# Kernel tuning notes

Measured on AMD Instinct MI355X. Metric: run time of the kernel, lower is better.

## Reference

```python
import jax, jax.numpy as jnp
import numpy as np

HIDDEN = 128
RHO = 5        # K // 2 with K = 10
J = 5
SCALE = 5.0


def setup_inputs() -> dict:
    key = jax.random.key(0)
    ks = jax.random.split(key, 16)
    B, N, D = 2, 4096, HIDDEN
    eigvs = jax.random.uniform(ks[0], (B, N, D), dtype=jnp.float32)  # eigenvalue encodings in [0,1)
    x = jax.random.normal(ks[1], (B, N, D), dtype=jnp.float32)
    U = jax.random.normal(ks[2], (B, N, N), dtype=jnp.float32) / np.sqrt(N)
    s = 1.0 / np.sqrt(D)
    return {
        "eigvs": eigvs, "x": x, "U": U,
        # Linear weights stored as [in, out] (already transposed vs torch)
        "Wa": jax.random.normal(ks[3], (D, RHO), dtype=jnp.float32) * s,
        "ba": jnp.zeros((RHO,), jnp.float32),
        "Wb": jax.random.normal(ks[4], (D, RHO), dtype=jnp.float32) * s,
        "bb": jnp.zeros((RHO,), jnp.float32),
        "Ws": jax.random.normal(ks[5], (D, J), dtype=jnp.float32) * s,
        "bs": jnp.zeros((J,), jnp.float32),
        "WS": jax.random.normal(ks[6], (D, D), dtype=jnp.float32) * s,
        "bS": jnp.zeros((D,), jnp.float32),
        "WM": jax.random.normal(ks[7], (J, D, D), dtype=jnp.float32) * s,
        "bM": jnp.zeros((J, D), jnp.float32),
        "Ww": jax.random.normal(ks[8], (D, D), dtype=jnp.float32) * s,
        "bw": jnp.zeros((D,), jnp.float32),
    }


def _generate_g(a, sx, rho):
    # a: [B, rho]; sx: [B, J, N, D] scaled eigenvalues. Even Chebyshev polys.
    T_odd = jnp.ones_like(sx)
    T_even = sx
    g = a[:, 0, None, None, None] * T_even
    for i in range(1, rho):
        T_odd = 2.0 * sx * T_even - T_odd
        T_even = 2.0 * sx * T_odd - T_even
        g = g + a[:, i, None, None, None] * T_even
    return g


def _generate_h(b, e, rho):
    # b: [B, rho]; e: [B, N, D]. Odd Chebyshev polys.
    T_odd = jnp.ones_like(e)
    T_even = e
    h = b[:, 0, None, None] * T_odd
    for i in range(1, rho):
        T_odd = 2.0 * e * T_even - T_odd
        T_even = 2.0 * e * T_odd - T_even
        h = h + b[:, i, None, None] * T_odd
    return h


def reference(eigvs, x, U, Wa, ba, Wb, bb, Ws, bs, WS, bS, WM, bM, Ww, bw):
    # Filter coefficients from pooled eigenvalue encodings
    a_tilde = (eigvs @ Wa + ba).mean(axis=-2)                      # [B, rho]
    b_tilde = (eigvs @ Wb + bb).mean(axis=-2)                      # [B, rho]
    scale_tilde = jax.nn.sigmoid((eigvs @ Ws + bs).mean(axis=-2)) * SCALE  # [B, J]

    h = _generate_h(b_tilde, eigvs, RHO)                           # [B, N, D] scaling filter
    sx = scale_tilde[:, :, None, None] * eigvs[:, None]            # [B, J, N, D]
    g = _generate_g(a_tilde, sx, RHO)                              # [B, J, N, D] wavelet filters

    # Spectral convolution: U diag(filter) U^T x, per channel
    xt = jnp.einsum('bmn,bmd->bnd', U, x)                          # U^T x
    y_h = jnp.einsum('bnm,bmd->bnd', U, h * xt)                    # [B, N, D]
    y_g = jnp.einsum('bnm,bjmd->bjnd', U, g * xt[:, None])         # [B, J, N, D]

    out = y_h @ WS + bS                                            # S_kernel
    out = out + jnp.einsum('bjnd,jde->bne', y_g, WM) + bM.sum(0)   # sum_j M_kernels[j]
    return out @ Ww + bw                                           # W
```

## Files before the change

### kernel.cpp

```cpp
#include <hip/hip_runtime.h>
#include <hip/hip_bf16.h>
#include <stdint.h>

typedef unsigned short u16;
typedef __attribute__((ext_vector_type(8))) short bf16x8;
typedef __attribute__((ext_vector_type(4))) float f32x4;
typedef __attribute__((ext_vector_type(4))) uint32_t u32x4;

__device__ inline u16 f2bf(float f) {
  union { float f; uint32_t u; } v; v.f = f;
  uint32_t u = v.u;
  u += 0x7FFFu + ((u >> 16) & 1u);
  return (u16)(u >> 16);
}

__device__ inline uint32_t pkbf(float a, float b) {
  union { __hip_bfloat162 h; uint32_t u; } c;
  c.h = __float22bfloat162_rn(float2{a, b});
  return c.u;
}

__device__ inline void gl_lds16(const void* g, void* s) {
  __builtin_amdgcn_global_load_lds(
      (const __attribute__((address_space(1))) void*)(uintptr_t)(g),
      (__attribute__((address_space(3))) void*)(uint32_t)(uintptr_t)(s),
      16, 0, 0);
}

__global__ void k_mean(const float* __restrict__ eig, float* __restrict__ part) {
  const int b = blockIdx.y, chunk = blockIdx.x;
  const int t = threadIdx.x, d = t & 127, half = t >> 7;
  const float* p = eig + ((long)b * 4096 + chunk * 128 + half) * 128 + d;
  float s = 0.0f;
  for (int i = 0; i < 64; i++) s += p[(long)i * 256];
  __shared__ float red[256];
  red[t] = s;
  __syncthreads();
  if (t < 128) part[((long)b * 32 + chunk) * 128 + d] = red[t] + red[t + 128];
}

__global__ void k_coeff(const float* __restrict__ part,
                        const float* __restrict__ Wa, const float* __restrict__ ba,
                        const float* __restrict__ Wb, const float* __restrict__ bb_,
                        const float* __restrict__ Ws, const float* __restrict__ bs,
                        float* __restrict__ coeff) {
  const int b = blockIdx.x, t = threadIdx.x;
  __shared__ float sd[128];
  float s = 0.0f;
  for (int c = 0; c < 32; c++) s += part[((long)b * 32 + c) * 128 + t];
  sd[t] = s * (1.0f / 4096.0f);
  __syncthreads();
  if (t >= 15) return;
  const int kind = t / 5, r = t % 5;
  const float* W = (kind == 0) ? Wa : ((kind == 1) ? Wb : Ws);
  float v = 0.0f;
  for (int d = 0; d < 128; d++) v += sd[d] * W[d * 5 + r];
  v += (kind == 0) ? ba[r] : ((kind == 1) ? bb_[r] : bs[r]);
  if (kind == 2) v = 5.0f / (1.0f + __expf(-v));
  coeff[b * 16 + kind * 5 + r] = v;
}

__global__ void k_fold(const float* __restrict__ WS, const float* __restrict__ WM,
                       const float* __restrict__ Ww, const float* __restrict__ bS,
                       const float* __restrict__ bM, const float* __restrict__ bw,
                       u16* __restrict__ VT, float* __restrict__ cvec) {
  const int q = blockIdx.x;
  const int e = threadIdx.x;
  if (q == 768) {
    float s = bw[e];
    for (int k = 0; k < 128; k++) {
      float t = bS[k];
#pragma unroll
      for (int j = 0; j < 5; j++) t += bM[j * 128 + k];
      s += t * Ww[k * 128 + e];
    }
    cvec[e] = s;
    return;
  }
  const int f = q >> 7, d = q & 127;
  const float* Frow = (f == 0) ? (WS + d * 128) : (WM + ((long)(f - 1) * 128 + d) * 128);
  float s = 0.0f;
  for (int k = 0; k < 128; k++) s += Frow[k] * Ww[k * 128 + e];
  VT[(long)e * 768 + f * 128 + d] = f2bf(s);
}

__global__ void k_filter(const float* __restrict__ eig, const float* __restrict__ xs,
                         const float* __restrict__ coeff, u16* __restrict__ Mod) {
  const int b = blockIdx.y;
  const int n = blockIdx.x * 2 + (threadIdx.x >> 7);
  const int d = threadIdx.x & 127;
  const long ridx = (long)b * 4096 + n;
  const long off = ridx * 128 + d;
  const float e = eig[off];
  float xv = 0.0f;
#pragma unroll
  for (int s = 0; s < 8; s++) xv += xs[off + (long)s * 1048576];
  const float* cf = coeff + b * 16;
  float To = 1.0f, Tev = e;
  float h = cf[5];
#pragma unroll
  for (int i = 1; i < 5; i++) {
    To = 2.0f * e * Tev - To;
    Tev = 2.0f * e * To - Tev;
    h += cf[5 + i] * To;
  }
  u16* row = Mod + ridx * 768;
  row[d] = f2bf(h * xv);
#pragma unroll
  for (int j = 0; j < 5; j++) {
    const float sx = cf[10 + j] * e;
    float To2 = 1.0f, Te2 = sx;
    float g = cf[0] * Te2;
#pragma unroll
    for (int i = 1; i < 5; i++) {
      To2 = 2.0f * sx * Te2 - To2;
      Te2 = 2.0f * sx * To2 - Te2;
      g += cf[i] * Te2;
    }
    row[(j + 1) * 128 + d] = f2bf(g * xv);
  }
}

__global__ void k_wred(const float* __restrict__ wsl, u16* __restrict__ wT) {
  const long i = ((long)blockIdx.x * 256 + threadIdx.x) * 4;
  float4 s = *(const float4*)(wsl + i);
#pragma unroll
  for (int k = 1; k < 4; k++) {
    const float4 t = *(const float4*)(wsl + i + (long)k * 1048576);
    s.x += t.x; s.y += t.y; s.z += t.z; s.w += t.w;
  }
  uint32_t lo = pkbf(s.x, s.y), hi = pkbf(s.z, s.w);
  *(uint2*)(wT + i) = uint2{lo, hi};
}

__global__ void k_outred(const float* __restrict__ os, const float* __restrict__ cvec,
                         float* __restrict__ out) {
  const long i = (long)blockIdx.x * 256 + threadIdx.x;
  float4 r = *(const float4*)(os + 4 * i);
#pragma unroll
  for (int s = 1; s < 8; s++) {
    const float4 t = *(const float4*)(os + 4 * i + (long)s * 1048576);
    r.x += t.x; r.y += t.y; r.z += t.z; r.w += t.w;
  }
  const float4 cv = *(const float4*)(cvec + (i & 31) * 4);
  r.x += cv.x; r.y += cv.y; r.z += cv.z; r.w += cv.w;
  *(float4*)(out + 4 * i) = r;
}

__device__ inline void stage_t32(const float* __restrict__ srcK, int lda,
                                 u16* __restrict__ lds, int t) {
  const int q = t & 15, cb = t >> 4;
  const float* r0 = srcK + (long)(2 * q) * lda + cb * 8;
  const float* r1 = r0 + lda;
  const float4 a0 = *(const float4*)(r0);
  const float4 a1 = *(const float4*)(r0 + 4);
  const float4 b0 = *(const float4*)(r1);
  const float4 b1 = *(const float4*)(r1 + 4);
  uint32_t* d = (uint32_t*)lds;
  const int base = cb * 128 + q;
  d[base +   0] = pkbf(a0.x, b0.x);
  d[base +  16] = pkbf(a0.y, b0.y);
  d[base +  32] = pkbf(a0.z, b0.z);
  d[base +  48] = pkbf(a0.w, b0.w);
  d[base +  64] = pkbf(a1.x, b1.x);
  d[base +  80] = pkbf(a1.y, b1.y);
  d[base +  96] = pkbf(a1.z, b1.z);
  d[base + 112] = pkbf(a1.w, b1.w);
}

template <int AT, int BT>
__global__ __launch_bounds__(256) void k_gemm(
    const void* __restrict__ A, long sA, int lda,
    const void* __restrict__ B, long sB, int ldb,
    float* __restrict__ C, long sC, int ldc, long kslice,
    int K, int kchunk, int m_tiles) {
  __shared__ __align__(16) u16 As[128 * 32];
  __shared__ __align__(16) u16 Bs[128 * 32];
  const int bb = blockIdx.z, ks = blockIdx.y;
  const int tm = blockIdx.x % m_tiles, tn = blockIdx.x / m_tiles;
  const int tid = threadIdx.x, wave = tid >> 6, lane = tid & 63;
  const int wm = (wave >> 1) * 64, wn = (wave & 1) * 64;
  f32x4 acc[4][4];
#pragma unroll
  for (int i = 0; i < 4; i++)
#pragma unroll
    for (int j = 0; j < 4; j++)
#pragma unroll
      for (int r = 0; r < 4; r++) acc[i][j][r] = 0.0f;
  const int a_off = (wm + (lane & 15)) * 64 + (lane >> 4) * 16;
  const int b_off = (wn + (lane & 15)) * 64 + (lane >> 4) * 16;
  const int srow = wave * 32 + (lane >> 2);
  const int scol = (lane & 3) * 8;
  for (int k0 = 0; k0 < kchunk; k0 += 32) {
    const int kb = ks * kchunk + k0;
    if constexpr (AT == 0) {
      const u16* Ab = (const u16*)A + (long)bb * sA + (long)tm * 128 * lda + kb;
#pragma unroll
      for (int i = 0; i < 2; i++)
        gl_lds16(Ab + (long)(srow + i * 16) * lda + scol,
                 (char*)As + (wave * 32 + i * 16) * 64);
    } else if constexpr (AT == 1) {
      const float* src = (const float*)A + (long)bb * sA +
                         (long)(tm * 128 + (tid >> 1)) * lda + kb + (tid & 1) * 16;
      const float4 f0 = *(const float4*)(src);
      const float4 f1 = *(const float4*)(src + 4);
      const float4 f2 = *(const float4*)(src + 8);
      const float4 f3 = *(const float4*)(src + 12);
      u32x4* dst = (u32x4*)((char*)As + (tid >> 1) * 64 + (tid & 1) * 32);
      dst[0] = u32x4{pkbf(f0.x, f0.y), pkbf(f0.z, f0.w), pkbf(f1.x, f1.y), pkbf(f1.z, f1.w)};
      dst[1] = u32x4{pkbf(f2.x, f2.y), pkbf(f2.z, f2.w), pkbf(f3.x, f3.y), pkbf(f3.z, f3.w)};
    } else {
      const float* src = (const float*)A + (long)bb * sA + (long)kb * lda + tm * 128;
      stage_t32(src, lda, As, tid);
    }
    if constexpr (BT == 0) {
      const u16* Bb = (const u16*)B + (long)bb * sB + (long)tn * 128 * ldb + kb;
#pragma unroll
      for (int i = 0; i < 2; i++)
        gl_lds16(Bb + (long)(srow + i * 16) * ldb + scol,
                 (char*)Bs + (wave * 32 + i * 16) * 64);
    } else {
      const float* src = (const float*)B + (long)bb * sB + (long)kb * ldb + tn * 128;
      stage_t32(src, ldb, Bs, tid);
    }
    __syncthreads();
    bf16x8 af[4], bfr[4];
#pragma unroll
    for (int mt = 0; mt < 4; mt++)
      af[mt] = *(const bf16x8*)((const char*)As + a_off + mt * 1024);
#pragma unroll
    for (int nt = 0; nt < 4; nt++)
      bfr[nt] = *(const bf16x8*)((const char*)Bs + b_off + nt * 1024);
#pragma unroll
    for (int mt = 0; mt < 4; mt++)
#pragma unroll
      for (int nt = 0; nt < 4; nt++)
        acc[mt][nt] = __builtin_amdgcn_mfma_f32_16x16x32_bf16(af[mt], bfr[nt], acc[mt][nt], 0, 0, 0);
    __syncthreads();
  }
  const int lr = (lane >> 4) * 4, lc = lane & 15;
  float* Cf = C + (long)bb * sC + (long)ks * kslice;
#pragma unroll
  for (int mt = 0; mt < 4; mt++)
#pragma unroll
    for (int nt = 0; nt < 4; nt++) {
      const int col = tn * 128 + wn + nt * 16 + lc;
#pragma unroll
      for (int r = 0; r < 4; r++) {
        const int row = tm * 128 + wm + mt * 16 + lr + r;
        Cf[(long)row * ldc + col] = acc[mt][nt][r];
      }
    }
}

extern "C" void kernel_launch(void* const* d_in, const int* in_sizes, int n_in,
                              void* d_out, int out_size, void* d_ws, size_t ws_size,
                              hipStream_t stream) {
  const float* eig = (const float*)d_in[0];
  const float* x   = (const float*)d_in[1];
  const float* U   = (const float*)d_in[2];
  const float* Wa  = (const float*)d_in[3];
  const float* ba  = (const float*)d_in[4];
  const float* Wb  = (const float*)d_in[5];
  const float* bb  = (const float*)d_in[6];
  const float* Ws  = (const float*)d_in[7];
  const float* bs  = (const float*)d_in[8];
  const float* WSm = (const float*)d_in[9];
  const float* bS  = (const float*)d_in[10];
  const float* WM  = (const float*)d_in[11];
  const float* bM  = (const float*)d_in[12];
  const float* Ww  = (const float*)d_in[13];
  const float* bw  = (const float*)d_in[14];

  char* ws = (char*)d_ws;
  float* xs   = (float*)(ws + 0);
  u16*   Mod  = (u16*)(ws + 33554432);
  u16*   VT   = (u16*)(ws + 46137344);
  float* wsl  = (float*)(ws + 46333952);
  u16*   wT   = (u16*)(ws + 63111168);
  float* os   = (float*)(ws + 65208320);
  float* part = (float*)(ws + 98762752);
  float* coef = (float*)(ws + 98795520);
  float* cvec = (float*)(ws + 98795648);
  float* outp = (float*)d_out;

  if (ws_size < (size_t)98796160) return;

  k_mean<<<dim3(32, 2), 256, 0, stream>>>(eig, part);
  k_coeff<<<2, 128, 0, stream>>>(part, Wa, ba, Wb, bb, Ws, bs, coef);

  k_fold<<<769, 128, 0, stream>>>(WSm, WM, Ww, bS, bM, bw, VT, cvec);

  k_gemm<2, 2><<<dim3(32, 8, 2), 256, 0, stream>>>(
      U, 16777216L, 4096, x, 524288L, 128,
      xs, 524288L, 128, 1048576L, 4096, 512, 32);

  k_filter<<<dim3(2048, 2), 256, 0, stream>>>(eig, xs, coef, Mod);

  k_gemm<0, 0><<<dim3(32, 4, 2), 256, 0, stream>>>(
      VT, 0L, 768, Mod, 3145728L, 768,
      wsl, 524288L, 4096, 1048576L, 768, 192, 1);
  k_wred<<<1024, 256, 0, stream>>>(wsl, wT);

  k_gemm<1, 0><<<dim3(32, 8, 2), 256, 0, stream>>>(
      U, 16777216L, 4096, wT, 524288L, 4096,
      os, 524288L, 128, 1048576L, 4096, 512, 32);

  k_outred<<<1024, 256, 0, stream>>>(os, cvec, outp);
}
```

Baseline: 319.9 us.

## Pre-transpose x to bf16, read U row-major, drop split-K reduction and merge prep kernels

Adds a prep kernel that computes eigenvalue partial means and transposes x into bf16, so the first U^T x GEMM reads U as a row-major B operand through a padded LDS layout and writes its result transposed. The filter-weight GEMM drops split-K and writes bf16 directly, which removes the separate reduction kernel and its fp32 workspace traffic. The coefficient and weight-fold kernels are merged into one launch. The aim is fewer launches and less intermediate memory traffic, at the cost of lower parallelism in the unsplit GEMM.

```diff
diff --git a/kernel.cpp b/kernel.cpp
--- a/kernel.cpp
+++ b/kernel.cpp
@@ -27,45 +27,84 @@
       16, 0, 0);
 }
 
-__global__ void k_mean(const float* __restrict__ eig, float* __restrict__ part) {
-  const int b = blockIdx.y, chunk = blockIdx.x;
-  const int t = threadIdx.x, d = t & 127, half = t >> 7;
-  const float* p = eig + ((long)b * 4096 + chunk * 128 + half) * 128 + d;
-  float s = 0.0f;
-  for (int i = 0; i < 64; i++) s += p[(long)i * 256];
-  __shared__ float red[256];
-  red[t] = s;
+__global__ __launch_bounds__(256) void k_pre(const float* __restrict__ eig,
+                                             const float* __restrict__ x,
+                                             float* __restrict__ part,
+                                             u16* __restrict__ xT) {
+  const int bid = blockIdx.x, t = threadIdx.x;
+  if (bid < 64) {
+    const int b = bid >> 5, chunk = bid & 31;
+    const int d = t & 127, half = t >> 7;
+    const float* p = eig + ((long)b * 4096 + chunk * 128 + half) * 128 + d;
+    float s = 0.0f;
+    for (int i = 0; i < 64; i++) s += p[(long)i * 256];
+    __shared__ float red[256];
+    red[t] = s;
+    __syncthreads();
+    if (t < 128) part[((long)b * 32 + chunk) * 128 + d] = red[t] + red[t + 128];
+    return;
+  }
+  const int q = bid - 64;
+  const int b = q >> 7, rem = q & 127;
+  const int tr = rem & 63, tc = rem >> 6;
+  const float* I = x + (long)b * 524288;
+  u16* O = xT + (long)b * 524288;
+  __shared__ uint32_t L[64][33];
+  const int r = t >> 2, cq = (t & 3) * 4;
+  const float* src = I + (long)(tr * 64 + r) * 128 + tc * 64;
+#pragma unroll
+  for (int i = 0; i < 4; i++) {
+    const float4 f = *(const float4*)(src + cq + 16 * i);
+    const int c = cq + 16 * i;
+    L[r][(c >> 1)]     = pkbf(f.x, f.y);
+    L[r][(c >> 1) + 1] = pkbf(f.z, f.w);
+  }
   __syncthreads();
-  if (t < 128) part[((long)b * 32 + chunk) * 128 + d] = red[t] + red[t + 128];
-}
-
-__global__ void k_coeff(const float* __restrict__ part,
-                        const float* __restrict__ Wa, const float* __restrict__ ba,
-                        const float* __restrict__ Wb, const float* __restrict__ bb_,
-                        const float* __restrict__ Ws, const float* __restrict__ bs,
-                        float* __restrict__ coeff) {
-  const int b = blockIdx.x, t = threadIdx.x;
-  __shared__ float sd[128];
-  float s = 0.0f;
-  for (int c = 0; c < 32; c++) s += part[((long)b * 32 + c) * 128 + t];
-  sd[t] = s * (1.0f / 4096.0f);
-  __syncthreads();
-  if (t >= 15) return;
-  const int kind = t / 5, r = t % 5;
-  const float* W = (kind == 0) ? Wa : ((kind == 1) ? Wb : Ws);
-  float v = 0.0f;
-  for (int d = 0; d < 128; d++) v += sd[d] * W[d * 5 + r];
-  v += (kind == 0) ? ba[r] : ((kind == 1) ? bb_[r] : bs[r]);
-  if (kind == 2) v = 5.0f / (1.0f + __expf(-v));
-  coeff[b * 16 + kind * 5 + r] = v;
-}
-
-__global__ void k_fold(const float* __restrict__ WS, const float* __restrict__ WM,
-                       const float* __restrict__ Ww, const float* __restrict__ bS,
-                       const float* __restrict__ bM, const float* __restrict__ bw,
-                       u16* __restrict__ VT, float* __restrict__ cvec) {
-  const int q = blockIdx.x;
-  const int e = threadIdx.x;
+  const int r0 = (t & 7) * 8;
+#pragma unroll
+  for (int p = 0; p < 2; p++) {
+    const int c = (t >> 3) + 32 * p;
+    uint32_t w[4];
+#pragma unroll
+    for (int i = 0; i < 4; i++) {
+      const uint32_t w0 = L[r0 + 2 * i][c >> 1];
+      const uint32_t w1 = L[r0 + 2 * i + 1][c >> 1];
+      const u16 v0 = (c & 1) ? (u16)(w0 >> 16) : (u16)(w0 & 0xffff);
+      const u16 v1 = (c & 1) ? (u16)(w1 >> 16) : (u16)(w1 & 0xffff);
+      w[i] = (uint32_t)v0 | ((uint32_t)v1 << 16);
+    }
+    u32x4* dst = (u32x4*)(O + (long)(tc * 64 + c) * 4096 + tr * 64 + r0);
+    *dst = u32x4{w[0], w[1], w[2], w[3]};
+  }
+}
+
+__global__ void k_foldcoeff(const float* __restrict__ WS, const float* __restrict__ WM,
+                            const float* __restrict__ Ww, const float* __restrict__ bS,
+                            const float* __restrict__ bM, const float* __restrict__ bw,
+                            const float* __restrict__ part,
+                            const float* __restrict__ Wa, const float* __restrict__ ba,
+                            const float* __restrict__ Wb, const float* __restrict__ bb_,
+                            const float* __restrict__ Ws, const float* __restrict__ bs,
+                            u16* __restrict__ VT, float* __restrict__ cvec,
+                            float* __restrict__ coeff) {
+  const int q = blockIdx.x, e = threadIdx.x;
+  if (q >= 769) {
+    const int b = q - 769;
+    __shared__ float sd[128];
+    float s = 0.0f;
+    for (int c = 0; c < 32; c++) s += part[((long)b * 32 + c) * 128 + e];
+    sd[e] = s * (1.0f / 4096.0f);
+    __syncthreads();
+    if (e >= 15) return;
+    const int kind = e / 5, r = e % 5;
+    const float* W = (kind == 0) ? Wa : ((kind == 1) ? Wb : Ws);
+    float v = 0.0f;
+    for (int d = 0; d < 128; d++) v += sd[d] * W[d * 5 + r];
+    v += (kind == 0) ? ba[r] : ((kind == 1) ? bb_[r] : bs[r]);
+    if (kind == 2) v = 5.0f / (1.0f + __expf(-v));
+    coeff[b * 16 + kind * 5 + r] = v;
+    return;
+  }
   if (q == 768) {
     float s = bw[e];
     for (int k = 0; k < 128; k++) {
@@ -121,18 +160,6 @@
   }
 }
 
-__global__ void k_wred(const float* __restrict__ wsl, u16* __restrict__ wT) {
-  const long i = ((long)blockIdx.x * 256 + threadIdx.x) * 4;
-  float4 s = *(const float4*)(wsl + i);
-#pragma unroll
-  for (int k = 1; k < 4; k++) {
-    const float4 t = *(const float4*)(wsl + i + (long)k * 1048576);
-    s.x += t.x; s.y += t.y; s.z += t.z; s.w += t.w;
-  }
-  uint32_t lo = pkbf(s.x, s.y), hi = pkbf(s.z, s.w);
-  *(uint2*)(wT + i) = uint2{lo, hi};
-}
-
 __global__ void k_outred(const float* __restrict__ os, const float* __restrict__ cvec,
                          float* __restrict__ out) {
   const long i = (long)blockIdx.x * 256 + threadIdx.x;
@@ -147,35 +174,14 @@
   *(float4*)(out + 4 * i) = r;
 }
 
-__device__ inline void stage_t32(const float* __restrict__ srcK, int lda,
-                                 u16* __restrict__ lds, int t) {
-  const int q = t & 15, cb = t >> 4;
-  const float* r0 = srcK + (long)(2 * q) * lda + cb * 8;
-  const float* r1 = r0 + lda;
-  const float4 a0 = *(const float4*)(r0);
-  const float4 a1 = *(const float4*)(r0 + 4);
-  const float4 b0 = *(const float4*)(r1);
-  const float4 b1 = *(const float4*)(r1 + 4);
-  uint32_t* d = (uint32_t*)lds;
-  const int base = cb * 128 + q;
-  d[base +   0] = pkbf(a0.x, b0.x);
-  d[base +  16] = pkbf(a0.y, b0.y);
-  d[base +  32] = pkbf(a0.z, b0.z);
-  d[base +  48] = pkbf(a0.w, b0.w);
-  d[base +  64] = pkbf(a1.x, b1.x);
-  d[base +  80] = pkbf(a1.y, b1.y);
-  d[base +  96] = pkbf(a1.z, b1.z);
-  d[base + 112] = pkbf(a1.w, b1.w);
-}
-
-template <int AT, int BT>
+template <int AT, int BT, int CT>
 __global__ __launch_bounds__(256) void k_gemm(
     const void* __restrict__ A, long sA, int lda,
     const void* __restrict__ B, long sB, int ldb,
-    float* __restrict__ C, long sC, int ldc, long kslice,
+    void* __restrict__ C, long sC, int ldc, long kslice,
     int K, int kchunk, int m_tiles) {
   __shared__ __align__(16) u16 As[128 * 32];
-  __shared__ __align__(16) u16 Bs[128 * 32];
+  __shared__ __align__(16) u16 Bs[128 * 34 + 64];
   const int bb = blockIdx.z, ks = blockIdx.y;
   const int tm = blockIdx.x % m_tiles, tn = blockIdx.x / m_tiles;
   const int tid = threadIdx.x, wave = tid >> 6, lane = tid & 63;
@@ -188,7 +194,9 @@
 #pragma unroll
       for (int r = 0; r < 4; r++) acc[i][j][r] = 0.0f;
   const int a_off = (wm + (lane & 15)) * 64 + (lane >> 4) * 16;
-  const int b_off = (wn + (lane & 15)) * 64 + (lane >> 4) * 16;
+  const int b_off = (BT == 2) ? ((wn + (lane & 15)) * 68 + (lane >> 4) * 16)
+                              : ((wn + (lane & 15)) * 64 + (lane >> 4) * 16);
+  const int b_nt_stride = (BT == 2) ? 1088 : 1024;
   const int srow = wave * 32 + (lane >> 2);
   const int scol = (lane & 3) * 8;
   for (int k0 = 0; k0 < kchunk; k0 += 32) {
@@ -199,19 +207,18 @@
       for (int i = 0; i < 2; i++)
         gl_lds16(Ab + (long)(srow + i * 16) * lda + scol,
                  (char*)As + (wave * 32 + i * 16) * 64);
-    } else if constexpr (AT == 1) {
-      const float* src = (const float*)A + (long)bb * sA +
-                         (long)(tm * 128 + (tid >> 1)) * lda + kb + (tid & 1) * 16;
-      const float4 f0 = *(const float4*)(src);
-      const float4 f1 = *(const float4*)(src + 4);
-      const float4 f2 = *(const float4*)(src + 8);
-      const float4 f3 = *(const float4*)(src + 12);
-      u32x4* dst = (u32x4*)((char*)As + (tid >> 1) * 64 + (tid & 1) * 32);
-      dst[0] = u32x4{pkbf(f0.x, f0.y), pkbf(f0.z, f0.w), pkbf(f1.x, f1.y), pkbf(f1.z, f1.w)};
-      dst[1] = u32x4{pkbf(f2.x, f2.y), pkbf(f2.z, f2.w), pkbf(f3.x, f3.y), pkbf(f3.z, f3.w)};
     } else {
-      const float* src = (const float*)A + (long)bb * sA + (long)kb * lda + tm * 128;
-      stage_t32(src, lda, As, tid);
+      const float* Af = (const float*)A + (long)bb * sA + (long)tm * 128 * lda + kb;
+      const float* s0 = Af + (long)(tid >> 2) * lda + (tid & 3) * 8;
+      const float4 f0 = *(const float4*)(s0);
+      const float4 f1 = *(const float4*)(s0 + 4);
+      *(u32x4*)((char*)As + tid * 16) =
+          u32x4{pkbf(f0.x, f0.y), pkbf(f0.z, f0.w), pkbf(f1.x, f1.y), pkbf(f1.z, f1.w)};
+      const float* s1 = s0 + (long)64 * lda;
+      const float4 g0 = *(const float4*)(s1);
+      const float4 g1 = *(const float4*)(s1 + 4);
+      *(u32x4*)((char*)As + 4096 + tid * 16) =
+          u32x4{pkbf(g0.x, g0.y), pkbf(g0.z, g0.w), pkbf(g1.x, g1.y), pkbf(g1.z, g1.w)};
     }
     if constexpr (BT == 0) {
       const u16* Bb = (const u16*)B + (long)bb * sB + (long)tn * 128 * ldb + kb;
@@ -220,8 +227,24 @@
         gl_lds16(Bb + (long)(srow + i * 16) * ldb + scol,
                  (char*)Bs + (wave * 32 + i * 16) * 64);
     } else {
-      const float* src = (const float*)B + (long)bb * sB + (long)kb * ldb + tn * 128;
-      stage_t32(src, ldb, Bs, tid);
+      const int q = tid & 15, cb = tid >> 4;
+      const float* r0 = (const float*)B + (long)bb * sB + (long)(kb + 2 * q) * ldb +
+                        tn * 128 + cb * 8;
+      const float* r1 = r0 + ldb;
+      const float4 a0 = *(const float4*)(r0);
+      const float4 a1 = *(const float4*)(r0 + 4);
+      const float4 c0 = *(const float4*)(r1);
+      const float4 c1 = *(const float4*)(r1 + 4);
+      uint32_t* dw = (uint32_t*)Bs;
+      const int base = (cb * 8) * 17 + q;
+      dw[base + 0 * 17] = pkbf(a0.x, c0.x);
+      dw[base + 1 * 17] = pkbf(a0.y, c0.y);
+      dw[base + 2 * 17] = pkbf(a0.z, c0.z);
+      dw[base + 3 * 17] = pkbf(a0.w, c0.w);
+      dw[base + 4 * 17] = pkbf(a1.x, c1.x);
+      dw[base + 5 * 17] = pkbf(a1.y, c1.y);
+      dw[base + 6 * 17] = pkbf(a1.z, c1.z);
+      dw[base + 7 * 17] = pkbf(a1.w, c1.w);
     }
     __syncthreads();
     bf16x8 af[4], bfr[4];
@@ -230,7 +253,7 @@
       af[mt] = *(const bf16x8*)((const char*)As + a_off + mt * 1024);
 #pragma unroll
     for (int nt = 0; nt < 4; nt++)
-      bfr[nt] = *(const bf16x8*)((const char*)Bs + b_off + nt * 1024);
+      bfr[nt] = *(const bf16x8*)((const char*)Bs + b_off + nt * b_nt_stride);
 #pragma unroll
     for (int mt = 0; mt < 4; mt++)
 #pragma unroll
@@ -239,18 +262,46 @@
     __syncthreads();
   }
   const int lr = (lane >> 4) * 4, lc = lane & 15;
-  float* Cf = C + (long)bb * sC + (long)ks * kslice;
-#pragma unroll
-  for (int mt = 0; mt < 4; mt++)
-#pragma unroll
-    for (int nt = 0; nt < 4; nt++) {
-      const int col = tn * 128 + wn + nt * 16 + lc;
-#pragma unroll
-      for (int r = 0; r < 4; r++) {
-        const int row = tm * 128 + wm + mt * 16 + lr + r;
-        Cf[(long)row * ldc + col] = acc[mt][nt][r];
+  if constexpr (CT == 1) {
+    u16* Cb = (u16*)C + (long)bb * sC;
+#pragma unroll
+    for (int mt = 0; mt < 4; mt++)
+#pragma unroll
+      for (int nt = 0; nt < 4; nt++) {
+        const int col = tn * 128 + wn + nt * 16 + lc;
+#pragma unroll
+        for (int r = 0; r < 4; r++) {
+          const int row = tm * 128 + wm + mt * 16 + lr + r;
+          Cb[(long)row * ldc + col] = f2bf(acc[mt][nt][r]);
+        }
       }
-    }
+  } else if constexpr (CT == 0) {
+    float* Cf = (float*)C + (long)bb * sC + (long)ks * kslice;
+#pragma unroll
+    for (int mt = 0; mt < 4; mt++)
+#pragma unroll
+      for (int nt = 0; nt < 4; nt++) {
+        const int col = tn * 128 + wn + nt * 16 + lc;
+#pragma unroll
+        for (int r = 0; r < 4; r++) {
+          const int row = tm * 128 + wm + mt * 16 + lr + r;
+          Cf[(long)row * ldc + col] = acc[mt][nt][r];
+        }
+      }
+  } else {
+    float* Cf = (float*)C + (long)bb * sC + (long)ks * kslice;
+#pragma unroll
+    for (int mt = 0; mt < 4; mt++)
+#pragma unroll
+      for (int nt = 0; nt < 4; nt++) {
+        const int col = tn * 128 + wn + nt * 16 + lc;
+#pragma unroll
+        for (int r = 0; r < 4; r++) {
+          const int row = tm * 128 + wm + mt * 16 + lr + r;
+          Cf[(long)col * ldc + row] = acc[mt][nt][r];
+        }
+      }
+  }
 }
 
 extern "C" void kernel_launch(void* const* d_in, const int* in_sizes, int n_in,
@@ -274,37 +325,35 @@
 
   char* ws = (char*)d_ws;
   float* xs   = (float*)(ws + 0);
+  float* os   = (float*)(ws + 0);
   u16*   Mod  = (u16*)(ws + 33554432);
-  u16*   VT   = (u16*)(ws + 46137344);
-  float* wsl  = (float*)(ws + 46333952);
-  u16*   wT   = (u16*)(ws + 63111168);
-  float* os   = (float*)(ws + 65208320);
-  float* part = (float*)(ws + 98762752);
-  float* coef = (float*)(ws + 98795520);
-  float* cvec = (float*)(ws + 98795648);
+  u16*   xT   = (u16*)(ws + 46137344);
+  u16*   wT   = (u16*)(ws + 48234496);
+  u16*   VT   = (u16*)(ws + 50331648);
+  float* part = (float*)(ws + 50528256);
+  float* coef = (float*)(ws + 50561024);
+  float* cvec = (float*)(ws + 50561152);
   float* outp = (float*)d_out;
 
-  if (ws_size < (size_t)98796160) return;
-
-  k_mean<<<dim3(32, 2), 256, 0, stream>>>(eig, part);
-  k_coeff<<<2, 128, 0, stream>>>(part, Wa, ba, Wb, bb, Ws, bs, coef);
-
-  k_fold<<<769, 128, 0, stream>>>(WSm, WM, Ww, bS, bM, bw, VT, cvec);
-
-  k_gemm<2, 2><<<dim3(32, 8, 2), 256, 0, stream>>>(
-      U, 16777216L, 4096, x, 524288L, 128,
-      xs, 524288L, 128, 1048576L, 4096, 512, 32);
+  if (ws_size < (size_t)50561664) return;
+
+  k_pre<<<320, 256, 0, stream>>>(eig, x, part, xT);
+  k_foldcoeff<<<771, 128, 0, stream>>>(WSm, WM, Ww, bS, bM, bw, part,
+                                       Wa, ba, Wb, bb, Ws, bs, VT, cvec, coef);
+
+  k_gemm<0, 2, 2><<<dim3(32, 8, 2), 256, 0, stream>>>(
+      xT, 524288L, 4096, U, 16777216L, 4096,
+      (void*)xs, 524288L, 128, 1048576L, 4096, 512, 1);
 
   k_filter<<<dim3(2048, 2), 256, 0, stream>>>(eig, xs, coef, Mod);
 
-  k_gemm<0, 0><<<dim3(32, 4, 2), 256, 0, stream>>>(
+  k_gemm<0, 0, 1><<<dim3(32, 1, 2), 256, 0, stream>>>(
       VT, 0L, 768, Mod, 3145728L, 768,
-      wsl, 524288L, 4096, 1048576L, 768, 192, 1);
-  k_wred<<<1024, 256, 0, stream>>>(wsl, wT);
-
-  k_gemm<1, 0><<<dim3(32, 8, 2), 256, 0, stream>>>(
+      (void*)wT, 524288L, 4096, 0L, 768, 768, 1);
+
+  k_gemm<1, 0, 0><<<dim3(32, 8, 2), 256, 0, stream>>>(
       U, 16777216L, 4096, wT, 524288L, 4096,
-      os, 524288L, 128, 1048576L, 4096, 512, 32);
+      (void*)os, 524288L, 128, 1048576L, 4096, 512, 32);
 
   k_outred<<<1024, 256, 0, stream>>>(os, cvec, outp);
 }
```

New measurement: 312.8 us. 2.2% less time.
